# Performance work log

Measured on AMD Instinct MI355X. Metric: run time of the kernel, lower is better.

The kernel has to match this reference:

```python
import jax, jax.numpy as jnp
import numpy as np

B, C, FULLBIN, T = 4, 2, 1025, 1024
BINS = 1024            # n_fft // 2
BANDS = 4
D = BINS // BANDS      # 256
FF = 2048
FF2, FF4 = FF // 2, FF // 4
CROP = 1024
EPS = 1e-5


def layernorm(x, g, b):
    m = jnp.mean(x, axis=-1, keepdims=True)
    v = jnp.mean(jnp.square(x - m), axis=-1, keepdims=True)
    return (x - m) * jax.lax.rsqrt(v + EPS) * g + b


def dconv(x, w, pad):
    # depthwise Conv1d: x (B, Cc, L), w (Cc, 1, K)
    return jax.lax.conv_general_dilated(
        x, w, window_strides=(1,), padding=[(pad, pad)],
        feature_group_count=x.shape[1],
        dimension_numbers=('NCH', 'OIH', 'NCH'))


def pconv(x, w):
    # pointwise Conv1d: x (B, Ci, L), w (Co, Ci, 1)
    return jnp.einsum('bcl,oc->bol', x, w[:, :, 0])


def reference(src, in_w, ln1_g, ln1_b, glu_w, ln2_g, ln2_b,
              c1L_dw, c1L_pw, c1R_dw, c1R_pw, ln3_g, ln3_b,
              c1M_dw, c1M_pw, ln4_g, ln4_b,
              q_w, q_b, qc_w, qc_b, k_w, k_b, v_w, v_b, o_w, o_b, er,
              ln5_g, ln5_b, c2_w, c3_w, out_w):
    s = src[:, :, :BINS]                                 # (B,C,F,T)
    x = jnp.einsum('bcft,c->btf', s, in_w[0])            # in_project + squeeze -> (B,T,BINS)

    # GLU block
    h = layernorm(x, ln1_g, ln1_b)
    g = h @ glu_w.T                                       # (B,T,2*BINS)
    x = x + g[..., :BINS] * jax.nn.sigmoid(g[..., BINS:])

    # conv feed-forward (note: conv1L applied without transpose, as in original)
    h = layernorm(x, ln2_g, ln2_b)
    hL = jax.nn.relu(pconv(dconv(h, c1L_dw, 5), c1L_pw))                          # (B,FF2,BINS)
    hR = jax.nn.relu(pconv(dconv(jnp.swapaxes(h, 1, 2), c1R_dw, 3), c1R_pw))      # (B,FF4,T)
    hR = jnp.swapaxes(hR, 1, 2)                                                   # (B,T,FF4)
    hR = jnp.pad(hR, ((0, 0), (0, 0), (0, BINS - FF4)))
    h = layernorm(hL + hR, ln3_g, ln3_b)                                          # (B,FF2,BINS)
    h = pconv(dconv(jnp.swapaxes(h, 1, 2), c1M_dw, 3), c1M_pw)                    # (B,BINS,FF2)
    x = x + jnp.swapaxes(h, 1, 2)

    # multiband frame attention (q_conv reused for q,k,v as in original)
    h = layernorm(x, ln4_g, ln4_b)

    def qkv(W, bvec):
        y = h @ W.T + bvec
        y = dconv(jnp.swapaxes(y, 1, 2), qc_w, 3) + qc_b[None, :, None]
        return jnp.swapaxes(y, 1, 2).reshape(B, T, BANDS, D)

    q = qkv(q_w, q_b).transpose(0, 2, 1, 3)              # (B,BANDS,T,D)
    k = qkv(k_w, k_b).transpose(0, 2, 3, 1)              # (B,BANDS,D,T)
    v = qkv(v_w, v_b).transpose(0, 2, 1, 3)              # (B,BANDS,T,D)

    p = jnp.pad(q @ er, ((0, 0), (0, 0), (0, 0), (1, 0)))  # (B,BANDS,T,CROP+1)
    p = jnp.swapaxes(p, 2, 3)[:, :, 1:, :]                 # (B,BANDS,CROP,T)
    qk = (q @ k + p) / jnp.sqrt(jnp.float32(BINS))
    a = jax.nn.softmax(qk, axis=-1)
    o = (a @ v).transpose(0, 2, 1, 3).reshape(B, T, BINS) @ o_w.T + o_b
    x = x + o

    # squared-ReLU MLP
    h = layernorm(x, ln5_g, ln5_b)
    h = jnp.square(jax.nn.relu(h @ c2_w.T)) @ c3_w.T
    x = x + h

    # stack back as extra channel, output head, ReLU1, replicate-pad freq row
    t = jnp.swapaxes(x, 1, 2)[:, None]                   # (B,1,BINS,T)
    s2 = jnp.concatenate([s, t], axis=1)                 # (B,C+1,BINS,T)
    y = jnp.einsum('bcft,oc->boft', s2, out_w)           # (B,2,BINS,T)
    y = jnp.clip(y, 0.0, 6.0) / 6.0
    return jnp.concatenate([y, y[:, :, -1:, :]], axis=2)  # (B,2,FULLBIN,T)


def setup_inputs() -> dict:
    key = jax.random.key(0)
    ks = jax.random.split(key, 20)
    n = lambda i, shape, s=0.02: jax.random.normal(ks[i], shape, jnp.float32) * s
    return {
        'src': jax.random.normal(ks[0], (B, C, FULLBIN, T), jnp.float32),
        'in_w': n(1, (1, C)),
        'ln1_g': jnp.ones((BINS,), jnp.float32), 'ln1_b': jnp.zeros((BINS,), jnp.float32),
        'glu_w': n(2, (2 * BINS, BINS)),
        'ln2_g': jnp.ones((BINS,), jnp.float32), 'ln2_b': jnp.zeros((BINS,), jnp.float32),
        'c1L_dw': n(3, (BINS, 1, 11), 0.1), 'c1L_pw': n(4, (FF2, BINS, 1)),
        'c1R_dw': n(5, (BINS, 1, 7), 0.1), 'c1R_pw': n(6, (FF4, BINS, 1)),
        'ln3_g': jnp.ones((FF2,), jnp.float32), 'ln3_b': jnp.zeros((FF2,), jnp.float32),
        'c1M_dw': n(7, (FF2, 1, 7), 0.1), 'c1M_pw': n(8, (BINS, FF2, 1)),
        'ln4_g': jnp.ones((BINS,), jnp.float32), 'ln4_b': jnp.zeros((BINS,), jnp.float32),
        'q_w': n(9, (BINS, BINS)), 'q_b': jnp.zeros((BINS,), jnp.float32),
        'qc_w': n(10, (BINS, 1, 7), 0.1), 'qc_b': jnp.zeros((BINS,), jnp.float32),
        'k_w': n(11, (BINS, BINS)), 'k_b': jnp.zeros((BINS,), jnp.float32),
        'v_w': n(12, (BINS, BINS)), 'v_b': jnp.zeros((BINS,), jnp.float32),
        'o_w': n(13, (BINS, BINS)), 'o_b': jnp.zeros((BINS,), jnp.float32),
        'er': jax.random.normal(ks[14], (D, CROP), jnp.float32),
        'ln5_g': jnp.ones((BINS,), jnp.float32), 'ln5_b': jnp.zeros((BINS,), jnp.float32),
        'c2_w': n(15, (FF, BINS)), 'c3_w': n(16, (BINS, FF)),
        'out_w': n(17, (2, C + 1)),
    }
```

## Files before the change

kernel.cpp:

```cpp
#include <hip/hip_runtime.h>
#include <math.h>


typedef unsigned short u16;
typedef __attribute__((ext_vector_type(4))) float floatx4;
typedef __attribute__((ext_vector_type(8))) short short8;

#define NB 4
static const long long M1 = 1024LL * 1024LL;

__device__ __forceinline__ float bf2f(u16 h) {
    union { unsigned int u; float f; } v;
    v.u = ((unsigned int)h) << 16;
    return v.f;
}
__device__ __forceinline__ u16 f2bf(float x) {
    union { float f; unsigned int u; } v;
    v.f = x;
    unsigned int r = (v.u + 0x7FFFu + ((v.u >> 16) & 1u)) >> 16;
    return (u16)r;
}

__device__ __forceinline__ void async_cp16(const u16* g, u16* lds) {
    __builtin_amdgcn_global_load_lds(
        (const __attribute__((address_space(1))) unsigned int*)g,
        (__attribute__((address_space(3))) unsigned int*)lds, 16, 0, 0);
}

__device__ __forceinline__ float block_sum(float v) {
    __shared__ float sd[4];
    #pragma unroll
    for (int off = 32; off; off >>= 1) v += __shfl_down(v, off, 64);
    int lane = threadIdx.x & 63, wid = threadIdx.x >> 6;
    __syncthreads();
    if (lane == 0) sd[wid] = v;
    __syncthreads();
    return sd[0] + sd[1] + sd[2] + sd[3];
}

template<int BM, int BN, int ACT, int OUT>
__global__ __launch_bounds__(256)
void gemm_bf(const u16* __restrict__ A, const u16* __restrict__ B,
             void* __restrict__ Cv, int K, int lda, int ldb, int ldc,
             long long sAz, long long sBz, long long sCz,
             const float* __restrict__ bias, float scale)
{
    constexpr int MI = BM / 32;
    constexpr int NJ = BN / 32;

    A += (long long)blockIdx.z * sAz;
    B += (long long)blockIdx.z * sBz;
    const long long zc = (long long)blockIdx.z * sCz;

    __shared__ u16 As[BM * 64];
    __shared__ u16 Bs[BN * 64];

    const int id = blockIdx.x + gridDim.x * blockIdx.y;
    const int bx = (id >> 3) % gridDim.x;
    const int by = (id & 7) + 8 * ((id >> 3) / gridDim.x);
    const int m0 = by * BM;
    const int n0 = bx * BN;

    const int lane = threadIdx.x & 63;
    const int w    = threadIdx.x >> 6;
    const int wm   = (w >> 1) * (BM / 2);
    const int wn   = (w & 1) * (BN / 2);
    const int srow = lane >> 2;
    const int scol = (lane & 3) * 8;

    floatx4 acc[MI][NJ];
    #pragma unroll
    for (int i = 0; i < MI; i++)
        #pragma unroll
        for (int j = 0; j < NJ; j++)
            acc[i][j] = floatx4{0.f, 0.f, 0.f, 0.f};

    for (int k0 = 0; k0 < K; k0 += 64) {
        #pragma unroll
        for (int r = 0; r < BM / 32; r++) {
            const int inst = w * (BM / 32) + r;
            const int rg = inst >> 1, kb = inst & 1;
            async_cp16(A + (long long)(m0 + rg * 16 + srow) * lda + k0 + kb * 32 + scol,
                       &As[(rg * 2 + kb) * 512]);
        }
        #pragma unroll
        for (int r = 0; r < BN / 32; r++) {
            const int inst = w * (BN / 32) + r;
            const int rg = inst >> 1, kb = inst & 1;
            async_cp16(B + (long long)(n0 + rg * 16 + srow) * ldb + k0 + kb * 32 + scol,
                       &Bs[(rg * 2 + kb) * 512]);
        }
        __syncthreads();

        #pragma unroll
        for (int s = 0; s < 2; s++) {
            short8 a[MI], b[NJ];
            const int fr = lane & 15;
            const int q  = lane >> 4;
            const int go = (fr * 4 + q) * 8;
            #pragma unroll
            for (int i = 0; i < MI; i++)
                a[i] = *(const short8*)&As[(((wm >> 4) + i) * 2 + s) * 512 + go];
            #pragma unroll
            for (int j = 0; j < NJ; j++)
                b[j] = *(const short8*)&Bs[(((wn >> 4) + j) * 2 + s) * 512 + go];
            #pragma unroll
            for (int i = 0; i < MI; i++)
                #pragma unroll
                for (int j = 0; j < NJ; j++)
                    acc[i][j] = __builtin_amdgcn_mfma_f32_16x16x32_bf16(
                        a[i], b[j], acc[i][j], 0, 0, 0);
        }
        __syncthreads();
    }

    float* Cf = (float*)Cv;
    u16*  Cb  = (u16*)Cv;
    const int cn    = n0 + wn + (lane & 15);
    const int rbase = m0 + wm + (lane >> 4) * 4;
    float bj[NJ];
    #pragma unroll
    for (int j = 0; j < NJ; j++) bj[j] = bias ? bias[cn + j * 16] : 0.f;

    #pragma unroll
    for (int i = 0; i < MI; i++) {
        #pragma unroll
        for (int r = 0; r < 4; r++) {
            const int m = rbase + i * 16 + r;
            #pragma unroll
            for (int j = 0; j < NJ; j++) {
                const int n = cn + j * 16;
                float v = (acc[i][j][r] + bj[j]) * scale;
                if (ACT == 1) v = fmaxf(v, 0.f);
                else if (ACT == 2) { v = fmaxf(v, 0.f); v = v * v; }
                const long long ci = zc + (long long)m * ldc + n;
                if (OUT == 0)      Cf[ci] = v;
                else if (OUT == 1) Cf[ci] += v;
                else if (OUT == 2) Cb[ci] = f2bf(v);
                else               Cb[ci] = f2bf(bf2f(Cb[ci]) + v);
            }
        }
    }
}

__global__ __launch_bounds__(256)
void glugemm_k(const u16* __restrict__ A, const u16* __restrict__ B1,
               const u16* __restrict__ B2, u16* __restrict__ X)
{
    constexpr int BM = 128, BN = 64, MI = 4, NJ = 2;
    __shared__ u16 As[BM * 64];
    __shared__ u16 B1s[BN * 64];
    __shared__ u16 B2s[BN * 64];

    const int id = blockIdx.x + gridDim.x * blockIdx.y;
    const int bx = (id >> 3) % gridDim.x;
    const int by = (id & 7) + 8 * ((id >> 3) / gridDim.x);
    const int m0 = by * BM;
    const int n0 = bx * BN;

    const int lane = threadIdx.x & 63;
    const int w    = threadIdx.x >> 6;
    const int wm   = (w >> 1) * 64;
    const int wn   = (w & 1) * 32;
    const int srow = lane >> 2;
    const int scol = (lane & 3) * 8;

    floatx4 acc1[MI][NJ], acc2[MI][NJ];
    #pragma unroll
    for (int i = 0; i < MI; i++)
        #pragma unroll
        for (int j = 0; j < NJ; j++) {
            acc1[i][j] = floatx4{0.f, 0.f, 0.f, 0.f};
            acc2[i][j] = floatx4{0.f, 0.f, 0.f, 0.f};
        }

    for (int k0 = 0; k0 < 1024; k0 += 64) {
        #pragma unroll
        for (int r = 0; r < 4; r++) {
            const int inst = w * 4 + r;
            const int rg = inst >> 1, kb = inst & 1;
            async_cp16(A + (long long)(m0 + rg * 16 + srow) * 1024 + k0 + kb * 32 + scol,
                       &As[(rg * 2 + kb) * 512]);
        }
        #pragma unroll
        for (int r = 0; r < 2; r++) {
            const int inst = w * 2 + r;
            const int rg = inst >> 1, kb = inst & 1;
            async_cp16(B1 + (long long)(n0 + rg * 16 + srow) * 1024 + k0 + kb * 32 + scol,
                       &B1s[(rg * 2 + kb) * 512]);
            async_cp16(B2 + (long long)(n0 + rg * 16 + srow) * 1024 + k0 + kb * 32 + scol,
                       &B2s[(rg * 2 + kb) * 512]);
        }
        __syncthreads();

        #pragma unroll
        for (int s = 0; s < 2; s++) {
            short8 a[MI], b1[NJ], b2[NJ];
            const int fr = lane & 15;
            const int q  = lane >> 4;
            const int go = (fr * 4 + q) * 8;
            #pragma unroll
            for (int i = 0; i < MI; i++)
                a[i] = *(const short8*)&As[(((wm >> 4) + i) * 2 + s) * 512 + go];
            #pragma unroll
            for (int j = 0; j < NJ; j++) {
                b1[j] = *(const short8*)&B1s[(((wn >> 4) + j) * 2 + s) * 512 + go];
                b2[j] = *(const short8*)&B2s[(((wn >> 4) + j) * 2 + s) * 512 + go];
            }
            #pragma unroll
            for (int i = 0; i < MI; i++)
                #pragma unroll
                for (int j = 0; j < NJ; j++) {
                    acc1[i][j] = __builtin_amdgcn_mfma_f32_16x16x32_bf16(
                        a[i], b1[j], acc1[i][j], 0, 0, 0);
                    acc2[i][j] = __builtin_amdgcn_mfma_f32_16x16x32_bf16(
                        a[i], b2[j], acc2[i][j], 0, 0, 0);
                }
        }
        __syncthreads();
    }

    const int cn    = n0 + wn + (lane & 15);
    const int rbase = m0 + wm + (lane >> 4) * 4;
    #pragma unroll
    for (int i = 0; i < MI; i++)
        #pragma unroll
        for (int r = 0; r < 4; r++) {
            const int m = rbase + i * 16 + r;
            #pragma unroll
            for (int j = 0; j < NJ; j++) {
                const int n = cn + j * 16;
                float g = acc1[i][j][r] / (1.f + __expf(-acc2[i][j][r]));
                u16* xp = &X[(long long)m * 1024 + n];
                *xp = f2bf(bf2f(*xp) + g);
            }
        }
}

#define SGEMM_MMA_STEP                                                        \
    __syncthreads();                                                          \
    _Pragma("unroll")                                                         \
    for (int s = 0; s < 2; s++) {                                             \
        short8 a[MI], b[NJ];                                                  \
        const int fr = lane & 15;                                             \
        const int q  = lane >> 4;                                             \
        const int go = (fr * 4 + q) * 8;                                      \
        _Pragma("unroll")                                                     \
        for (int i = 0; i < MI; i++)                                          \
            a[i] = *(const short8*)&As[(((wm >> 4) + i) * 2 + s) * 512 + go]; \
        _Pragma("unroll")                                                     \
        for (int j = 0; j < NJ; j++)                                          \
            b[j] = *(const short8*)&Bs[(((wn >> 4) + j) * 2 + s) * 512 + go]; \
        _Pragma("unroll")                                                     \
        for (int i = 0; i < MI; i++)                                          \
            _Pragma("unroll")                                                 \
            for (int j = 0; j < NJ; j++)                                      \
                acc[i][j] = __builtin_amdgcn_mfma_f32_16x16x32_bf16(          \
                    a[i], b[j], acc[i][j], 0, 0, 0);                          \
    }                                                                         \
    __syncthreads();

__global__ __launch_bounds__(256)
void sgemm_exp_k(const u16* __restrict__ Qpk, const u16* __restrict__ Kpk,
                 const u16* __restrict__ ErT,
                 u16* __restrict__ S, float* __restrict__ rowsum, float scale)
{
    constexpr int MI = 4, NJ = 4;
    const int i0 = blockIdx.x;
    const int x  = i0 & 7;
    const int j0 = i0 >> 3;
    const int z  = x + 8 * (j0 & 1);
    const int t  = j0 >> 1;
    const int bx = t & 7, by = t >> 3;

    const u16* Aq = Qpk + (long long)z * 262144;
    const u16* Bk = Kpk + (long long)z * 262144;
    S += (long long)z * M1;
    rowsum += z << 10;

    __shared__ u16 As[128 * 64];
    __shared__ u16 Bs[128 * 64];

    const int m0 = by * 128;
    const int n0 = bx * 128;

    const int lane = threadIdx.x & 63;
    const int w    = threadIdx.x >> 6;
    const int wm   = (w >> 1) * 64;
    const int wn   = (w & 1) * 64;
    const int srow = lane >> 2;
    const int scol = (lane & 3) * 8;

    floatx4 acc[MI][NJ];
    #pragma unroll
    for (int i = 0; i < MI; i++)
        #pragma unroll
        for (int j = 0; j < NJ; j++)
            acc[i][j] = floatx4{0.f, 0.f, 0.f, 0.f};

    for (int k0 = 0; k0 < 256; k0 += 64) {
        #pragma unroll
        for (int r = 0; r < 4; r++) {
            const int inst = w * 4 + r;
            const int rg = inst >> 1, kb = inst & 1;
            const int cb = k0 + kb * 32;
            async_cp16(Aq + (long long)(m0 + rg * 16 + srow) * 256 + cb + scol,
                       &As[(rg * 2 + kb) * 512]);
            async_cp16(Bk + (long long)(n0 + rg * 16 + srow) * 256 + cb + scol,
                       &Bs[(rg * 2 + kb) * 512]);
        }
        SGEMM_MMA_STEP
    }
    for (int k0 = 0; k0 < 256; k0 += 64) {
        #pragma unroll
        for (int r = 0; r < 4; r++) {
            const int inst = w * 4 + r;
            const int rg = inst >> 1, kb = inst & 1;
            const int cb = k0 + kb * 32;
            async_cp16(ErT + (long long)(m0 + rg * 16 + srow) * 256 + cb + scol,
                       &As[(rg * 2 + kb) * 512]);
            async_cp16(Aq + (long long)(n0 + rg * 16 + srow) * 256 + cb + scol,
                       &Bs[(rg * 2 + kb) * 512]);
        }
        SGEMM_MMA_STEP
    }

    const int cn    = n0 + wn + (lane & 15);
    const int rbase = m0 + wm + (lane >> 4) * 4;
    #pragma unroll
    for (int i = 0; i < MI; i++)
        #pragma unroll
        for (int r = 0; r < 4; r++) {
            const int m = rbase + i * 16 + r;
            float part = 0.f;
            #pragma unroll
            for (int j = 0; j < NJ; j++) {
                const int n = cn + j * 16;
                float e = __expf(acc[i][j][r] * scale);
                S[(long long)m * 1024 + n] = f2bf(e);
                part += e;
            }
            #pragma unroll
            for (int off = 8; off; off >>= 1) part += __shfl_xor(part, off, 64);
            if ((lane & 15) == 0) atomicAdd(&rowsum[m], part);
        }
}

__global__ __launch_bounds__(256)
void aogemm_k(const u16* __restrict__ Sb, const u16* __restrict__ Vt,
              const float* __restrict__ rowsum, u16* __restrict__ AO)
{
    constexpr int MI = 4, NJ = 2;
    const int i0 = blockIdx.x;
    const int x  = i0 & 7;
    const int j0 = i0 >> 3;
    const int z  = x + 8 * (j0 & 1);
    const int t  = j0 >> 1;
    const int bx = t & 3, by = t >> 2;

    Sb += (long long)z * M1;
    Vt += (long long)z * 262144;
    rowsum += z << 10;
    const long long zc = (long long)(z >> 2) * M1 + (z & 3) * 256;

    __shared__ u16 As[128 * 64];
    __shared__ u16 Bs[64 * 64];

    const int m0 = by * 128;
    const int n0 = bx * 64;

    const int lane = threadIdx.x & 63;
    const int w    = threadIdx.x >> 6;
    const int wm   = (w >> 1) * 64;
    const int wn   = (w & 1) * 32;
    const int srow = lane >> 2;
    const int scol = (lane & 3) * 8;

    floatx4 acc[MI][NJ];
    #pragma unroll
    for (int i = 0; i < MI; i++)
        #pragma unroll
        for (int j = 0; j < NJ; j++)
            acc[i][j] = floatx4{0.f, 0.f, 0.f, 0.f};

    for (int k0 = 0; k0 < 1024; k0 += 64) {
        #pragma unroll
        for (int r = 0; r < 4; r++) {
            const int inst = w * 4 + r;
            const int rg = inst >> 1, kb = inst & 1;
            async_cp16(Sb + (long long)(m0 + rg * 16 + srow) * 1024 + k0 + kb * 32 + scol,
                       &As[(rg * 2 + kb) * 512]);
        }
        #pragma unroll
        for (int r = 0; r < 2; r++) {
            const int inst = w * 2 + r;
            const int rg = inst >> 1, kb = inst & 1;
            async_cp16(Vt + (long long)(n0 + rg * 16 + srow) * 1024 + k0 + kb * 32 + scol,
                       &Bs[(rg * 2 + kb) * 512]);
        }
        SGEMM_MMA_STEP
    }

    const int cn    = n0 + wn + (lane & 15);
    const int rbase = m0 + wm + (lane >> 4) * 4;
    #pragma unroll
    for (int i = 0; i < MI; i++)
        #pragma unroll
        for (int r = 0; r < 4; r++) {
            const int m = rbase + i * 16 + r;
            const float inv = 1.f / rowsum[m];
            #pragma unroll
            for (int j = 0; j < NJ; j++) {
                const int n = cn + j * 16;
                AO[zc + (long long)m * 1024 + n] = f2bf(acc[i][j][r] * inv);
            }
        }
}

__global__ __launch_bounds__(256)
void ln_bf_k(const u16* __restrict__ in, u16* __restrict__ out,
             const float* __restrict__ g, const float* __restrict__ b)
{
    long long row = blockIdx.x;
    int tid = threadIdx.x;
    ushort4 u = ((const ushort4*)(in + (row << 10)))[tid];
    float x0 = bf2f(u.x), x1 = bf2f(u.y), x2 = bf2f(u.z), x3 = bf2f(u.w);
    float s = x0 + x1 + x2 + x3;
    s = block_sum(s);
    float mean = s * (1.f / 1024.f);
    float dx = x0 - mean, dy = x1 - mean, dz = x2 - mean, dw = x3 - mean;
    float s2 = dx * dx + dy * dy + dz * dz + dw * dw;
    s2 = block_sum(s2);
    float inv = rsqrtf(s2 * (1.f / 1024.f) + 1e-5f);
    float4 gg = ((const float4*)g)[tid];
    float4 bb = ((const float4*)b)[tid];
    ushort4 o;
    o.x = f2bf(dx * inv * gg.x + bb.x);
    o.y = f2bf(dy * inv * gg.y + bb.y);
    o.z = f2bf(dz * inv * gg.z + bb.z);
    o.w = f2bf(dw * inv * gg.w + bb.w);
    ((ushort4*)(out + (row << 10)))[tid] = o;
}

__device__ __forceinline__ void dconv7_vec8(
    const u16* __restrict__ in, u16* __restrict__ out,
    const float* __restrict__ wtr, int gidx)
{
    const int f8 = (gidx & 127) * 8;
    const int bt = gidx >> 7;
    const int t  = bt & 1023;
    const long long rowbase = (long long)(bt - t) * 1024;
    float acc[8] = {0.f, 0.f, 0.f, 0.f, 0.f, 0.f, 0.f, 0.f};
    #pragma unroll
    for (int k = 0; k < 7; k++) {
        int tt = t + k - 3;
        if (tt >= 0 && tt < 1024) {
            short8 v = *(const short8*)&in[rowbase + (long long)tt * 1024 + f8];
            float4 wa = *(const float4*)&wtr[k * 1024 + f8];
            float4 wb = *(const float4*)&wtr[k * 1024 + f8 + 4];
            acc[0] += bf2f((u16)v[0]) * wa.x;
            acc[1] += bf2f((u16)v[1]) * wa.y;
            acc[2] += bf2f((u16)v[2]) * wa.z;
            acc[3] += bf2f((u16)v[3]) * wa.w;
            acc[4] += bf2f((u16)v[4]) * wb.x;
            acc[5] += bf2f((u16)v[5]) * wb.y;
            acc[6] += bf2f((u16)v[6]) * wb.z;
            acc[7] += bf2f((u16)v[7]) * wb.w;
        }
    }
    short8 o;
    #pragma unroll
    for (int i = 0; i < 8; i++) o[i] = (short)f2bf(acc[i]);
    *(short8*)&out[(long long)bt * 1024 + f8] = o;
}

struct CastArgs {
    const float* s[10];
    const float* er; const float* qb; const float* kb; const float* vb;
    const float* dwR; const float* dwM; const float* dwQ;
    u16* ert; float* qkvb; float* wtr;
};
__global__ __launch_bounds__(256)
void castin_k(CastArgs a, u16* __restrict__ dst,
              const float* __restrict__ src, const float* __restrict__ inw,
              u16* __restrict__ X)
{
    const int bid = blockIdx.x;
    if (bid < 24576) {
        const int sz[10] = {2097152, 1048576, 524288, 1048576, 1048576,
                            1048576, 1048576, 1048576, 2097152, 2097152};
        int seg = bid >> 11;
        int tid = (bid & 2047) * 256 + threadIdx.x;
        if (seg < 10) {
            int n = sz[seg];
            int base = 0;
            for (int i = 0; i < seg; i++) base += sz[i];
            int i4 = tid * 4;
            if (i4 >= n) return;
            float4 v = *(const float4*)(a.s[seg] + i4);
            ushort4 o;
            o.x = f2bf(v.x); o.y = f2bf(v.y); o.z = f2bf(v.z); o.w = f2bf(v.w);
            *(ushort4*)(dst + base + i4) = o;
        } else if (seg == 10) {
            if (tid < 262144) {
                int j = tid >> 8, d = tid & 255;
                a.ert[tid] = f2bf(a.er[d * 1024 + j]);
            }
        } else {
            if (tid < 1024) a.qkvb[tid] = a.qb[tid];
            else if (tid < 2048) a.qkvb[tid] = a.kb[tid - 1024];
            else if (tid < 3072) a.qkvb[tid] = a.vb[tid - 2048];
            else if (tid < 3072 + 21504) {
                int i = tid - 3072;
                int tbl = i / 7168, r = i - tbl * 7168;
                int k = r >> 10, f = r & 1023;
                const float* s = (tbl == 0) ? a.dwR : (tbl == 1) ? a.dwM : a.dwQ;
                a.wtr[tbl * 7168 + k * 1024 + f] = s[f * 7 + k];
            }
        }
    } else {
        __shared__ float tile[32][33];
        int ib = bid - 24576;
        int f0 = (ib & 31) * 32, t0 = ((ib >> 5) & 31) * 32, b = ib >> 10;
        int tx = threadIdx.x & 31, ty = threadIdx.x >> 5;
        float w0 = inw[0], w1 = inw[1];
        for (int r = ty; r < 32; r += 8) {
            int f = f0 + r, t = t0 + tx;
            float s0 = src[(((long long)b * 2 + 0) * 1025 + f) * 1024 + t];
            float s1 = src[(((long long)b * 2 + 1) * 1025 + f) * 1024 + t];
            tile[r][tx] = w0 * s0 + w1 * s1;
        }
        __syncthreads();
        for (int r = ty; r < 32; r += 8)
            X[((long long)b * 1024 + t0 + r) * 1024 + f0 + tx] = f2bf(tile[tx][r]);
    }
}

__global__ __launch_bounds__(256)
void dconvFT_k(const u16* __restrict__ in, u16* __restrict__ outT,
               const float* __restrict__ wtrT, u16* __restrict__ outF,
               const float* __restrict__ wF)
{
    const int bid = blockIdx.x;
    if (bid < 2048) {
        dconv7_vec8(in, outT, wtrT, bid * 256 + threadIdx.x);
    } else {
        __shared__ float itile[32][44];
        __shared__ float otile[32][33];
        int ib = bid - 2048;
        int f0 = (ib & 31) * 32, t0 = ((ib >> 5) & 31) * 32, b = ib >> 10;
        int tx = threadIdx.x & 31, ty = threadIdx.x >> 5;
        for (int r = ty; r < 32; r += 8)
            for (int c = tx; c < 42; c += 32) {
                int f = f0 - 5 + c;
                itile[r][c] = (f >= 0 && f < 1024)
                    ? bf2f(in[((long long)(b * 1024 + t0 + r)) * 1024 + f]) : 0.f;
            }
        __syncthreads();
        for (int r = ty; r < 32; r += 8) {
            const float* wr = wF + (t0 + r) * 11;
            float acc = 0.f;
            #pragma unroll
            for (int k = 0; k < 11; k++) acc += itile[r][tx + k] * wr[k];
            otile[tx][r] = acc;
        }
        __syncthreads();
        for (int r = ty; r < 32; r += 8)
            outF[((long long)(b * 1024 + f0 + r)) * 1024 + t0 + tx] = f2bf(otile[r][tx]);
    }
}

__global__ __launch_bounds__(256)
void dconvT_bf_k(const u16* __restrict__ in, u16* __restrict__ out,
                 const float* __restrict__ wtr)
{
    dconv7_vec8(in, out, wtr, blockIdx.x * 256 + threadIdx.x);
}

__global__ __launch_bounds__(256)
void qkvpack_k(const u16* __restrict__ T3, const float* __restrict__ w,
               const float* __restrict__ wtrQ, const float* __restrict__ bias,
               u16* __restrict__ Qpk, u16* __restrict__ Kpk,
               u16* __restrict__ Vt, float* __restrict__ rowsum)
{
    const int bid = blockIdx.x;
    if (bid < 2048) {
        const int gidx = bid * 256 + threadIdx.x;
        const int f8 = (gidx & 127) * 8;
        const int t  = (gidx >> 7) & 1023;
        const int b  = gidx >> 17;
        float4 b0 = *(const float4*)&bias[f8];
        float4 b1 = *(const float4*)&bias[f8 + 4];
        float aq[8] = {b0.x, b0.y, b0.z, b0.w, b1.x, b1.y, b1.z, b1.w};
        float ak[8] = {b0.x, b0.y, b0.z, b0.w, b1.x, b1.y, b1.z, b1.w};
        #pragma unroll
        for (int k = 0; k < 7; k++) {
            int tt = t + k - 3;
            if (tt >= 0 && tt < 1024) {
                const u16* row = T3 + ((long long)((b << 10) + tt)) * 3072 + f8;
                short8 vq = *(const short8*)&row[0];
                short8 vk = *(const short8*)&row[1024];
                float4 wa = *(const float4*)&wtrQ[k * 1024 + f8];
                float4 wb = *(const float4*)&wtrQ[k * 1024 + f8 + 4];
                aq[0] += bf2f((u16)vq[0]) * wa.x;  ak[0] += bf2f((u16)vk[0]) * wa.x;
                aq[1] += bf2f((u16)vq[1]) * wa.y;  ak[1] += bf2f((u16)vk[1]) * wa.y;
                aq[2] += bf2f((u16)vq[2]) * wa.z;  ak[2] += bf2f((u16)vk[2]) * wa.z;
                aq[3] += bf2f((u16)vq[3]) * wa.w;  ak[3] += bf2f((u16)vk[3]) * wa.w;
                aq[4] += bf2f((u16)vq[4]) * wb.x;  ak[4] += bf2f((u16)vk[4]) * wb.x;
                aq[5] += bf2f((u16)vq[5]) * wb.y;  ak[5] += bf2f((u16)vk[5]) * wb.y;
                aq[6] += bf2f((u16)vq[6]) * wb.z;  ak[6] += bf2f((u16)vk[6]) * wb.z;
                aq[7] += bf2f((u16)vq[7]) * wb.w;  ak[7] += bf2f((u16)vk[7]) * wb.w;
            }
        }
        const int band = f8 >> 8, d = f8 & 255, z = (b << 2) | band;
        const long long base = (long long)z * 262144 + t * 256 + d;
        short8 oq, ok;
        #pragma unroll
        for (int i = 0; i < 8; i++) {
            oq[i] = (short)f2bf(aq[i]);
            ok[i] = (short)f2bf(ak[i]);
        }
        *(short8*)&Qpk[base] = oq;
        *(short8*)&Kpk[base] = ok;
    } else if (bid < 6144) {
        __shared__ float itile[38][32];
        __shared__ float otile[32][33];
        int vb = bid - 2048;
        int f0 = (vb & 31) * 32, t0 = ((vb >> 5) & 31) * 32, b = vb >> 10;
        int tx = threadIdx.x & 31, ty = threadIdx.x >> 5;
        for (int i = threadIdx.x; i < 38 * 32; i += 256) {
            int r = i >> 5, c = i & 31;
            int t = t0 - 3 + r;
            itile[r][c] = (t >= 0 && t < 1024)
                ? bf2f(T3[((long long)(b * 1024 + t)) * 3072 + 2048 + f0 + c]) : 0.f;
        }
        __syncthreads();
        for (int r = ty; r < 32; r += 8) {
            const float* wr = w + (f0 + tx) * 7;
            float acc = bias[f0 + tx];
            #pragma unroll
            for (int k = 0; k < 7; k++) acc += itile[r + k][tx] * wr[k];
            otile[tx][r] = acc;
        }
        __syncthreads();
        for (int r = ty; r < 32; r += 8)
            Vt[((long long)(b * 1024 + f0 + r)) * 1024 + t0 + tx] = f2bf(otile[r][tx]);
    } else {
        int i = (bid - 6144) * 256 + threadIdx.x;
        rowsum[i] = 0.f;
    }
}

__global__ __launch_bounds__(256)
void out_k(const float* __restrict__ src, const u16* __restrict__ X,
           const float* __restrict__ ow, float* __restrict__ out)
{
    __shared__ float tile[32][33];
    int b = blockIdx.z;
    int f0 = blockIdx.y * 32, t0 = blockIdx.x * 32;
    for (int r = threadIdx.y; r < 32; r += 8)
        tile[r][threadIdx.x] = bf2f(X[((long long)b * 1024 + t0 + r) * 1024 + f0 + threadIdx.x]);
    __syncthreads();
    float w00 = ow[0], w01 = ow[1], w02 = ow[2];
    float w10 = ow[3], w11 = ow[4], w12 = ow[5];
    for (int r = threadIdx.y; r < 32; r += 8) {
        int f = f0 + r, t = t0 + threadIdx.x;
        float s0 = src[(((long long)b * 2 + 0) * 1025 + f) * 1024 + t];
        float s1 = src[(((long long)b * 2 + 1) * 1025 + f) * 1024 + t];
        float xv = tile[threadIdx.x][r];
        float v0 = fminf(fmaxf(w00 * s0 + w01 * s1 + w02 * xv, 0.f), 6.f) * (1.f / 6.f);
        float v1 = fminf(fmaxf(w10 * s0 + w11 * s1 + w12 * xv, 0.f), 6.f) * (1.f / 6.f);
        out[(((long long)b * 2 + 0) * 1025 + f) * 1024 + t] = v0;
        out[(((long long)b * 2 + 1) * 1025 + f) * 1024 + t] = v1;
        if (f == 1023) {
            out[(((long long)b * 2 + 0) * 1025 + 1024) * 1024 + t] = v0;
            out[(((long long)b * 2 + 1) * 1025 + 1024) * 1024 + t] = v1;
        }
    }
}

extern "C" void kernel_launch(void* const* d_in, const int* in_sizes, int n_in,
                              void* d_out, int out_size, void* d_ws, size_t ws_size,
                              hipStream_t stream)
{
    const float* src    = (const float*)d_in[0];
    const float* in_w   = (const float*)d_in[1];
    const float* ln1_g  = (const float*)d_in[2];
    const float* ln1_b  = (const float*)d_in[3];
    const float* glu_w  = (const float*)d_in[4];
    const float* ln2_g  = (const float*)d_in[5];
    const float* ln2_b  = (const float*)d_in[6];
    const float* c1L_dw = (const float*)d_in[7];
    const float* c1L_pw = (const float*)d_in[8];
    const float* c1R_dw = (const float*)d_in[9];
    const float* c1R_pw = (const float*)d_in[10];
    const float* ln3_g  = (const float*)d_in[11];
    const float* ln3_b  = (const float*)d_in[12];
    const float* c1M_dw = (const float*)d_in[13];
    const float* c1M_pw = (const float*)d_in[14];
    const float* ln4_g  = (const float*)d_in[15];
    const float* ln4_b  = (const float*)d_in[16];
    const float* q_w    = (const float*)d_in[17];
    const float* q_b    = (const float*)d_in[18];
    const float* qc_w   = (const float*)d_in[19];
    const float* qc_b   = (const float*)d_in[20];
    const float* k_w    = (const float*)d_in[21];
    const float* k_b    = (const float*)d_in[22];
    const float* v_w    = (const float*)d_in[23];
    const float* v_b    = (const float*)d_in[24];
    const float* o_w    = (const float*)d_in[25];
    const float* o_b    = (const float*)d_in[26];
    const float* er     = (const float*)d_in[27];
    const float* ln5_g  = (const float*)d_in[28];
    const float* ln5_b  = (const float*)d_in[29];
    const float* c2_w   = (const float*)d_in[30];
    const float* c3_w   = (const float*)d_in[31];
    const float* out_w  = (const float*)d_in[32];
    float* out = (float*)d_out;

    const size_t MB = 1ull << 20;
    if (ws_size < 162 * MB) return;
    char* wsb = (char*)d_ws;
    u16* X       = (u16*)(wsb + 0);
    u16* SB      = (u16*)(wsb + 8 * MB);
    float* rowsum= (float*)(wsb + 16 * MB);
    u16* Qpk     = (u16*)(wsb + 32 * MB);
    u16* Kpk     = (u16*)(wsb + 40 * MB);
    u16* Hbf     = (u16*)(wsb + 64 * MB);
    u16* T1bf    = (u16*)(wsb + 72 * MB);
    u16* T3      = (u16*)(wsb + 72 * MB);
    u16* AO      = (u16*)(wsb + 80 * MB);
    u16* T2bf    = (u16*)(wsb + 96 * MB);
    u16* Vt      = (u16*)(wsb + 96 * MB);
    u16* Sbf     = (u16*)(wsb + 104 * MB);
    u16* Gbf     = (u16*)(wsb + 104 * MB);
    u16* W0      = (u16*)(wsb + 136 * MB);

    u16* glu_wb  = W0;
    u16* c1L_pwb = W0 + 2097152;
    u16* c1R_pwb = W0 + 3145728;
    u16* c1M_pwb = W0 + 3670016;
    u16* qkv_wb  = W0 + 4718592;
    u16* o_wb    = W0 + 7864320;
    u16* c2_wb   = W0 + 8912896;
    u16* c3_wb   = W0 + 11010048;
    u16* ertb    = W0 + 13107200;
    float* qkvb  = (float*)(W0 + 13369344);
    float* wtrb  = qkvb + 3072;
    float* wtrR  = wtrb;
    float* wtrM  = wtrb + 7168;
    float* wtrQ  = wtrb + 14336;

    const dim3 blk256(256);
    const dim3 tgrid(32, 32, NB);
    const dim3 tblk(32, 8);

    CastArgs ca;
    ca.s[0] = glu_w;  ca.s[1] = c1L_pw; ca.s[2] = c1R_pw; ca.s[3] = c1M_pw;
    ca.s[4] = q_w;    ca.s[5] = k_w;    ca.s[6] = v_w;    ca.s[7] = o_w;
    ca.s[8] = c2_w;   ca.s[9] = c3_w;
    ca.er = er; ca.qb = q_b; ca.kb = k_b; ca.vb = v_b;
    ca.dwR = c1R_dw; ca.dwM = c1M_dw; ca.dwQ = qc_w;
    ca.ert = ertb; ca.qkvb = qkvb; ca.wtr = wtrb;
    castin_k<<<28672, blk256, 0, stream>>>(ca, W0, src, in_w, X);

    ln_bf_k<<<4096, blk256, 0, stream>>>(X, Hbf, ln1_g, ln1_b);
    glugemm_k<<<dim3(16, 32, 1), blk256, 0, stream>>>(
        Hbf, glu_wb, glu_wb + 1048576, X);
    ln_bf_k<<<4096, blk256, 0, stream>>>(X, Hbf, ln2_g, ln2_b);
    dconvFT_k<<<6144, blk256, 0, stream>>>(Hbf, T1bf, wtrR, T2bf, c1L_dw);
    gemm_bf<128, 64, 1, 2><<<dim3(16, 8, NB), blk256, 0, stream>>>(
        c1L_pwb, T2bf, SB, 1024, 1024, 1024, 1024, 0, M1, M1, nullptr, 1.f);
    gemm_bf<64, 64, 1, 3><<<dim3(8, 64, 1), blk256, 0, stream>>>(
        T1bf, c1R_pwb, SB, 1024, 1024, 1024, 1024, 0, 0, 0, nullptr, 1.f);
    ln_bf_k<<<4096, blk256, 0, stream>>>(SB, Hbf, ln3_g, ln3_b);
    dconvT_bf_k<<<2048, blk256, 0, stream>>>(Hbf, T1bf, wtrM);
    gemm_bf<128, 64, 0, 3><<<dim3(16, 32, 1), blk256, 0, stream>>>(
        T1bf, c1M_pwb, X, 1024, 1024, 1024, 1024, 0, 0, 0, nullptr, 1.f);
    ln_bf_k<<<4096, blk256, 0, stream>>>(X, Hbf, ln4_g, ln4_b);
    gemm_bf<128, 128, 0, 2><<<dim3(24, 32, 1), blk256, 0, stream>>>(
        Hbf, qkv_wb, T3, 1024, 1024, 1024, 3072, 0, 0, 0, qkvb, 1.f);
    qkvpack_k<<<6208, blk256, 0, stream>>>(T3, qc_w, wtrQ, qc_b, Qpk, Kpk, Vt, rowsum);
    sgemm_exp_k<<<1024, blk256, 0, stream>>>(Qpk, Kpk, ertb, Sbf, rowsum, 0.03125f);
    aogemm_k<<<512, blk256, 0, stream>>>(Sbf, Vt, rowsum, AO);
    gemm_bf<128, 64, 0, 3><<<dim3(16, 32, 1), blk256, 0, stream>>>(
        AO, o_wb, X, 1024, 1024, 1024, 1024, 0, 0, 0, o_b, 1.f);
    ln_bf_k<<<4096, blk256, 0, stream>>>(X, Hbf, ln5_g, ln5_b);
    gemm_bf<128, 128, 2, 2><<<dim3(16, 32, 1), blk256, 0, stream>>>(
        Hbf, c2_wb, Gbf, 1024, 1024, 1024, 2048, 0, 0, 0, nullptr, 1.f);
    gemm_bf<128, 64, 0, 3><<<dim3(16, 32, 1), blk256, 0, stream>>>(
        Gbf, c3_wb, X, 2048, 2048, 2048, 1024, 0, 0, 0, nullptr, 1.f);
    out_k<<<tgrid, tblk, 0, stream>>>(src, X, out_w, out);
}
```

Before: 510.6 us.

## Merge conv1L/conv1R pointwise GEMMs into one launch, fuse residual add into layernorm

```diff
diff --git a/kernel.cpp b/kernel.cpp
--- a/kernel.cpp
+++ b/kernel.cpp
@@ -261,6 +261,112 @@
     __syncthreads();
 
 __global__ __launch_bounds__(256)
+void c1lr_k(const u16* __restrict__ PW, const u16* __restrict__ T2,
+            const u16* __restrict__ T1, const u16* __restrict__ RW,
+            u16* __restrict__ SBL, u16* __restrict__ SBR)
+{
+    __shared__ u16 As[128 * 64];
+    __shared__ u16 Bs[64 * 64];
+    const int lane = threadIdx.x & 63;
+    const int w    = threadIdx.x >> 6;
+    const int srow = lane >> 2;
+    const int scol = (lane & 3) * 8;
+
+    if (blockIdx.x < 512) {
+        constexpr int MI = 4, NJ = 2;
+        const int z  = blockIdx.x >> 7;
+        const int id = blockIdx.x & 127;
+        const int bx = id >> 3, by = id & 7;
+        const int m0 = by * 128, n0 = bx * 64;
+        const u16* B = T2 + (long long)z * M1;
+        const int wm = (w >> 1) * 64;
+        const int wn = (w & 1) * 32;
+
+        floatx4 acc[MI][NJ];
+        #pragma unroll
+        for (int i = 0; i < MI; i++)
+            #pragma unroll
+            for (int j = 0; j < NJ; j++)
+                acc[i][j] = floatx4{0.f, 0.f, 0.f, 0.f};
+
+        for (int k0 = 0; k0 < 1024; k0 += 64) {
+            #pragma unroll
+            for (int r = 0; r < 4; r++) {
+                const int inst = w * 4 + r;
+                const int rg = inst >> 1, kb = inst & 1;
+                async_cp16(PW + (long long)(m0 + rg * 16 + srow) * 1024 + k0 + kb * 32 + scol,
+                           &As[(rg * 2 + kb) * 512]);
+            }
+            #pragma unroll
+            for (int r = 0; r < 2; r++) {
+                const int inst = w * 2 + r;
+                const int rg = inst >> 1, kb = inst & 1;
+                async_cp16(B + (long long)(n0 + rg * 16 + srow) * 1024 + k0 + kb * 32 + scol,
+                           &Bs[(rg * 2 + kb) * 512]);
+            }
+            SGEMM_MMA_STEP
+        }
+
+        const int cn    = n0 + wn + (lane & 15);
+        const int rbase = m0 + wm + (lane >> 4) * 4;
+        #pragma unroll
+        for (int i = 0; i < MI; i++)
+            #pragma unroll
+            for (int r = 0; r < 4; r++) {
+                const int m = rbase + i * 16 + r;
+                #pragma unroll
+                for (int j = 0; j < NJ; j++) {
+                    const int n = cn + j * 16;
+                    SBL[(long long)z * M1 + (long long)m * 1024 + n] =
+                        f2bf(fmaxf(acc[i][j][r], 0.f));
+                }
+            }
+    } else {
+        constexpr int MI = 2, NJ = 2;
+        const int id = blockIdx.x - 512;
+        const int bx = (id >> 3) & 7;
+        const int by = (id & 7) + 8 * (id >> 6);
+        const int m0 = by * 64, n0 = bx * 64;
+        const int wm = (w >> 1) * 32;
+        const int wn = (w & 1) * 32;
+
+        floatx4 acc[MI][NJ];
+        #pragma unroll
+        for (int i = 0; i < MI; i++)
+            #pragma unroll
+            for (int j = 0; j < NJ; j++)
+                acc[i][j] = floatx4{0.f, 0.f, 0.f, 0.f};
+
+        for (int k0 = 0; k0 < 1024; k0 += 64) {
+            #pragma unroll
+            for (int r = 0; r < 2; r++) {
+                const int inst = w * 2 + r;
+                const int rg = inst >> 1, kb = inst & 1;
+                async_cp16(T1 + (long long)(m0 + rg * 16 + srow) * 1024 + k0 + kb * 32 + scol,
+                           &As[(rg * 2 + kb) * 512]);
+                async_cp16(RW + (long long)(n0 + rg * 16 + srow) * 1024 + k0 + kb * 32 + scol,
+                           &Bs[(rg * 2 + kb) * 512]);
+            }
+            SGEMM_MMA_STEP
+        }
+
+        const int cn    = n0 + wn + (lane & 15);
+        const int rbase = m0 + wm + (lane >> 4) * 4;
+        #pragma unroll
+        for (int i = 0; i < MI; i++)
+            #pragma unroll
+            for (int r = 0; r < 4; r++) {
+                const int m = rbase + i * 16 + r;
+                #pragma unroll
+                for (int j = 0; j < NJ; j++) {
+                    const int n = cn + j * 16;
+                    SBR[(long long)m * 512 + n] = f2bf(fmaxf(acc[i][j][r], 0.f));
+                }
+            }
+    }
+}
+
+__global__ __launch_bounds__(256)
 void sgemm_exp_k(const u16* __restrict__ Qpk, const u16* __restrict__ Kpk,
                  const u16* __restrict__ ErT,
                  u16* __restrict__ S, float* __restrict__ rowsum, float scale)
@@ -442,6 +548,36 @@
     ((ushort4*)(out + (row << 10)))[tid] = o;
 }
 
+__global__ __launch_bounds__(256)
+void ln_add_bf_k(const u16* __restrict__ inL, const u16* __restrict__ inR,
+                 u16* __restrict__ out,
+                 const float* __restrict__ g, const float* __restrict__ b)
+{
+    long long row = blockIdx.x;
+    int tid = threadIdx.x;
+    ushort4 u = ((const ushort4*)(inL + (row << 10)))[tid];
+    float x0 = bf2f(u.x), x1 = bf2f(u.y), x2 = bf2f(u.z), x3 = bf2f(u.w);
+    if (tid < 128) {
+        ushort4 v = ((const ushort4*)(inR + (row << 9)))[tid];
+        x0 += bf2f(v.x); x1 += bf2f(v.y); x2 += bf2f(v.z); x3 += bf2f(v.w);
+    }
+    float s = x0 + x1 + x2 + x3;
+    s = block_sum(s);
+    float mean = s * (1.f / 1024.f);
+    float dx = x0 - mean, dy = x1 - mean, dz = x2 - mean, dw = x3 - mean;
+    float s2 = dx * dx + dy * dy + dz * dz + dw * dw;
+    s2 = block_sum(s2);
+    float inv = rsqrtf(s2 * (1.f / 1024.f) + 1e-5f);
+    float4 gg = ((const float4*)g)[tid];
+    float4 bb = ((const float4*)b)[tid];
+    ushort4 o;
+    o.x = f2bf(dx * inv * gg.x + bb.x);
+    o.y = f2bf(dy * inv * gg.y + bb.y);
+    o.z = f2bf(dz * inv * gg.z + bb.z);
+    o.w = f2bf(dw * inv * gg.w + bb.w);
+    ((ushort4*)(out + (row << 10)))[tid] = o;
+}
+
 __device__ __forceinline__ void dconv7_vec8(
     const u16* __restrict__ in, u16* __restrict__ out,
     const float* __restrict__ wtr, int gidx)
@@ -472,6 +608,10 @@
     #pragma unroll
     for (int i = 0; i < 8; i++) o[i] = (short)f2bf(acc[i]);
     *(short8*)&out[(long long)bt * 1024 + f8] = o;
+}
+
+__device__ __forceinline__ int xcd_chunk2048(int bid) {
+    return (bid & 7) * 256 + (bid >> 3);
 }
 
 struct CastArgs {
@@ -543,7 +683,7 @@
 {
     const int bid = blockIdx.x;
     if (bid < 2048) {
-        dconv7_vec8(in, outT, wtrT, bid * 256 + threadIdx.x);
+        dconv7_vec8(in, outT, wtrT, xcd_chunk2048(bid) * 256 + threadIdx.x);
     } else {
         __shared__ float itile[32][44];
         __shared__ float otile[32][33];
@@ -574,7 +714,7 @@
 void dconvT_bf_k(const u16* __restrict__ in, u16* __restrict__ out,
                  const float* __restrict__ wtr)
 {
-    dconv7_vec8(in, out, wtr, blockIdx.x * 256 + threadIdx.x);
+    dconv7_vec8(in, out, wtr, xcd_chunk2048(blockIdx.x) * 256 + threadIdx.x);
 }
 
 __global__ __launch_bounds__(256)
@@ -585,7 +725,7 @@
 {
     const int bid = blockIdx.x;
     if (bid < 2048) {
-        const int gidx = bid * 256 + threadIdx.x;
+        const int gidx = xcd_chunk2048(bid) * 256 + threadIdx.x;
         const int f8 = (gidx & 127) * 8;
         const int t  = (gidx >> 7) & 1023;
         const int b  = gidx >> 17;
@@ -724,6 +864,7 @@
     u16* X       = (u16*)(wsb + 0);
     u16* SB      = (u16*)(wsb + 8 * MB);
     float* rowsum= (float*)(wsb + 16 * MB);
+    u16* SBR     = (u16*)(wsb + 24 * MB);
     u16* Qpk     = (u16*)(wsb + 32 * MB);
     u16* Kpk     = (u16*)(wsb + 40 * MB);
     u16* Hbf     = (u16*)(wsb + 64 * MB);
@@ -769,11 +910,8 @@
         Hbf, glu_wb, glu_wb + 1048576, X);
     ln_bf_k<<<4096, blk256, 0, stream>>>(X, Hbf, ln2_g, ln2_b);
     dconvFT_k<<<6144, blk256, 0, stream>>>(Hbf, T1bf, wtrR, T2bf, c1L_dw);
-    gemm_bf<128, 64, 1, 2><<<dim3(16, 8, NB), blk256, 0, stream>>>(
-        c1L_pwb, T2bf, SB, 1024, 1024, 1024, 1024, 0, M1, M1, nullptr, 1.f);
-    gemm_bf<64, 64, 1, 3><<<dim3(8, 64, 1), blk256, 0, stream>>>(
-        T1bf, c1R_pwb, SB, 1024, 1024, 1024, 1024, 0, 0, 0, nullptr, 1.f);
-    ln_bf_k<<<4096, blk256, 0, stream>>>(SB, Hbf, ln3_g, ln3_b);
+    c1lr_k<<<1024, blk256, 0, stream>>>(c1L_pwb, T2bf, T1bf, c1R_pwb, SB, SBR);
+    ln_add_bf_k<<<4096, blk256, 0, stream>>>(SB, SBR, Hbf, ln3_g, ln3_b);
     dconvT_bf_k<<<2048, blk256, 0, stream>>>(Hbf, T1bf, wtrM);
     gemm_bf<128, 64, 0, 3><<<dim3(16, 32, 1), blk256, 0, stream>>>(
         T1bf, c1M_pwb, X, 1024, 1024, 1024, 1024, 0, 0, 0, nullptr, 1.f);
```

Result: no change. 504.0 us (-1.3%).
